# Performance work log

Measured on AMD Instinct MI355X. Metric: run time of the kernel, lower is better.

## Reference

```python
import jax, jax.numpy as jnp
import numpy as np

MODEL_DIM = 1024
NUM_HEADS = 8
DIM_PER_HEAD = MODEL_DIM // NUM_HEADS  # 128
BATCH = 4
NODE_LEN = 128  # must equal DIM_PER_HEAD (see v += relative_mul broadcast in source)
LN_EPS = 1e-5


def setup_inputs() -> dict:
    key0 = jax.random.key(0)
    ks = jax.random.split(key0, 16)
    def w(k, shape, s=0.02):
        return jax.random.normal(k, shape, dtype=jnp.float32) * s
    inp = {
        "key": jax.random.normal(ks[0], (BATCH, NODE_LEN, MODEL_DIM), dtype=jnp.float32),
        "value": jax.random.normal(ks[1], (BATCH, NODE_LEN, MODEL_DIM), dtype=jnp.float32),
        "query": jax.random.normal(ks[2], (BATCH, NODE_LEN, MODEL_DIM), dtype=jnp.float32),
        "relative_q": jax.random.normal(ks[3], (BATCH * NUM_HEADS, NODE_LEN, NODE_LEN, DIM_PER_HEAD), dtype=jnp.float32),
        "relative_v": jax.random.normal(ks[4], (BATCH * NUM_HEADS, NODE_LEN, NODE_LEN, DIM_PER_HEAD), dtype=jnp.float32),
        "Wq": w(ks[5], (MODEL_DIM, MODEL_DIM)), "bq": w(ks[6], (MODEL_DIM,)),
        "Wk": w(ks[7], (MODEL_DIM, MODEL_DIM)), "bk": w(ks[8], (MODEL_DIM,)),
        "Wv": w(ks[9], (MODEL_DIM, MODEL_DIM)), "bv": w(ks[10], (MODEL_DIM,)),
        "Wo": w(ks[11], (MODEL_DIM, MODEL_DIM)), "bo": w(ks[12], (MODEL_DIM,)),
        "ln_gamma": jnp.ones((MODEL_DIM,), dtype=jnp.float32),
        "ln_beta": jnp.zeros((MODEL_DIM,), dtype=jnp.float32),
    }
    return inp


def _relative_mul(x, rel):
    # x: [BH, L, d], rel: [BH, L, L, d] -> [BH, L, L]
    # result[b,i,j] = sum_d x[b,i,d] * rel[b,i,j,d]  (matches torch bmm chain)
    return jnp.einsum('bid,bijd->bij', x, rel)


def reference(key, value, query, relative_q, relative_v,
              Wq, bq, Wk, bk, Wv, bv, Wo, bo, ln_gamma, ln_beta):
    residual = query
    B = key.shape[0]
    H, d = NUM_HEADS, DIM_PER_HEAD

    k = key @ Wk.T + bk      # [B, L, model_dim]
    v = value @ Wv.T + bv
    q = query @ Wq.T + bq

    # faithful to torch .view(batch*heads, -1, dim_per_head): row-major reshape
    k = k.reshape(B * H, -1, d)  # [BH, L, d]
    v = v.reshape(B * H, -1, d)
    q = q.reshape(B * H, -1, d)

    # scale = (dim_per_head // num_heads) ** -0.5, as in source
    scale = (d // H) ** (-0.5)

    attn = jnp.einsum('bid,bjd->bij', q, k)           # [BH, L, L]
    attn = attn + _relative_mul(q, relative_q)
    attn = attn * scale
    attn = jax.nn.softmax(attn, axis=2)

    # source: v += relative_mul(v, relative_v); requires L == d
    v = v + _relative_mul(v, relative_v)              # [BH, L, d] (L == d)
    context = jnp.einsum('bij,bjd->bid', attn, v)     # [BH, L, d]
    context = context.reshape(B, -1, H * d)           # [B, L, model_dim]

    out = context @ Wo.T + bo
    out = out + residual
    mu = jnp.mean(out, axis=-1, keepdims=True)
    var = jnp.mean(jnp.square(out - mu), axis=-1, keepdims=True)
    out = (out - mu) * jax.lax.rsqrt(var + LN_EPS) * ln_gamma + ln_beta
    return (out, attn)
```

## Files before the change

### kernel.cpp

```cpp
#include <hip/hip_runtime.h>

#define MD 1024
#define L 128
#define LN_EPS 1e-5f

typedef __attribute__((ext_vector_type(8))) short bh8;
typedef __attribute__((ext_vector_type(4))) float fx4;
typedef __attribute__((ext_vector_type(4))) float f4;

__device__ __forceinline__ unsigned short f2bf(float x) {
  unsigned int u = __float_as_uint(x);
  u = (u + 0x7FFFu + ((u >> 16) & 1u)) >> 16;
  return (unsigned short)u;
}

__global__ __launch_bounds__(256) void cvt_bf16(
    const float* s0, const float* s1, const float* s2, const float* s3,
    const float* s4, const float* s5, const float* s6, unsigned short* d0,
    unsigned short* d1, unsigned short* d2, unsigned short* d3,
    unsigned short* d4, unsigned short* d5, unsigned short* d6) {
  const float* s;
  unsigned short* d;
  int n;
  switch (blockIdx.z) {
    case 0: s = s0; d = d0; n = 524288; break;
    case 1: s = s1; d = d1; n = 524288; break;
    case 2: s = s2; d = d2; n = 524288; break;
    case 3: s = s3; d = d3; n = 1048576; break;
    case 4: s = s4; d = d4; n = 1048576; break;
    case 5: s = s5; d = d5; n = 1048576; break;
    default: s = s6; d = d6; n = 1048576; break;
  }
  const int idx = (blockIdx.x * 256 + threadIdx.x) * 8;
  if (idx < n) {
    const float4 a = *(const float4*)&s[idx];
    const float4 b = *(const float4*)&s[idx + 4];
    uint4 o;
    o.x = (unsigned int)f2bf(a.x) | ((unsigned int)f2bf(a.y) << 16);
    o.y = (unsigned int)f2bf(a.z) | ((unsigned int)f2bf(a.w) << 16);
    o.z = (unsigned int)f2bf(b.x) | ((unsigned int)f2bf(b.y) << 16);
    o.w = (unsigned int)f2bf(b.z) | ((unsigned int)f2bf(b.w) << 16);
    *(uint4*)&d[idx] = o;
  }
}

__device__ __forceinline__ void mfma_gemm_body(
    const unsigned short* __restrict__ A, const unsigned short* __restrict__ W,
    const float* __restrict__ bias, float* __restrict__ out,
    unsigned short* __restrict__ outb) {
  __shared__ short As[64][40];
  __shared__ short Bs[64][40];
  const int t = threadIdx.x;
  const int row0 = blockIdx.x * 64;
  const int col0 = blockIdx.y * 64;
  const int l = t & 63;
  const int w = t >> 6;
  const int wr = (w >> 1) * 32;
  const int wc = (w & 1) * 32;
  const int srow = t >> 2;
  const int skg = (t & 3) * 8;
  const int fr = l & 15;
  const int fq = (l >> 4) * 8;

  fx4 z = {0.f, 0.f, 0.f, 0.f};
  fx4 acc[2][2];
  acc[0][0] = z; acc[0][1] = z; acc[1][0] = z; acc[1][1] = z;

  for (int k0 = 0; k0 < MD; k0 += 32) {
    const uint4 av = *(const uint4*)&A[(size_t)(row0 + srow) * MD + k0 + skg];
    const uint4 bv = *(const uint4*)&W[(size_t)(col0 + srow) * MD + k0 + skg];
    __syncthreads();
    *(uint4*)&As[srow][skg] = av;
    *(uint4*)&Bs[srow][skg] = bv;
    __syncthreads();
    const bh8 a0 = *(const bh8*)&As[wr + fr][fq];
    const bh8 a1 = *(const bh8*)&As[wr + 16 + fr][fq];
    const bh8 b0 = *(const bh8*)&Bs[wc + fr][fq];
    const bh8 b1 = *(const bh8*)&Bs[wc + 16 + fr][fq];
    acc[0][0] = __builtin_amdgcn_mfma_f32_16x16x32_bf16(a0, b0, acc[0][0], 0, 0, 0);
    acc[0][1] = __builtin_amdgcn_mfma_f32_16x16x32_bf16(a0, b1, acc[0][1], 0, 0, 0);
    acc[1][0] = __builtin_amdgcn_mfma_f32_16x16x32_bf16(a1, b0, acc[1][0], 0, 0, 0);
    acc[1][1] = __builtin_amdgcn_mfma_f32_16x16x32_bf16(a1, b1, acc[1][1], 0, 0, 0);
  }

  const int fq4 = (l >> 4) * 4;
#pragma unroll
  for (int m = 0; m < 2; m++)
#pragma unroll
    for (int n = 0; n < 2; n++) {
      const int col = col0 + wc + n * 16 + fr;
      const float bval = bias[col];
#pragma unroll
      for (int r = 0; r < 4; r++) {
        const int row = row0 + wr + m * 16 + fq4 + r;
        const float v = acc[m][n][r] + bval;
        if (out) out[(size_t)row * MD + col] = v;
        if (outb) outb[(size_t)row * MD + col] = f2bf(v);
      }
    }
}

__global__ __launch_bounds__(256) void qkv_mfma(
    const unsigned short* Aq, const unsigned short* Ak,
    const unsigned short* Av, const unsigned short* Wq,
    const unsigned short* Wk, const unsigned short* Wv, const float* bq,
    const float* bk, const float* bv, float* qo, float* ko, float* vo,
    unsigned short* qb, unsigned short* kb) {
  if (blockIdx.z == 0) mfma_gemm_body(Aq, Wq, bq, qo, qb);
  else if (blockIdx.z == 1) mfma_gemm_body(Ak, Wk, bk, ko, kb);
  else mfma_gemm_body(Av, Wv, bv, vo, nullptr);
}

__global__ __launch_bounds__(256) void o_mfma(const unsigned short* A,
                                              const unsigned short* W,
                                              const float* bias, float* out) {
  mfma_gemm_body(A, W, bias, out, nullptr);
}

__global__ __launch_bounds__(256) void qk_mfma(const unsigned short* __restrict__ qb,
                                               const unsigned short* __restrict__ kb,
                                               float* __restrict__ S1) {
  __shared__ short Qs[128][40];
  __shared__ short Ks[128][40];
  const int g = blockIdx.x;
  const int t = threadIdx.x;
  const int l = t & 63;
  const int w = t >> 6;
  const unsigned short* qg = qb + (size_t)g * 16384;
  const unsigned short* kg = kb + (size_t)g * 16384;
  const int srow = t >> 1;
  const int sh = (t & 1) * 16;
  const int fr = l & 15;
  const int fq = (l >> 4) * 8;

  fx4 z = {0.f, 0.f, 0.f, 0.f};
  fx4 acc[2][8];
#pragma unroll
  for (int m = 0; m < 2; m++)
#pragma unroll
    for (int n = 0; n < 8; n++) acc[m][n] = z;

  for (int d0 = 0; d0 < 128; d0 += 32) {
    const size_t off = (size_t)srow * 128 + d0 + sh;
    const uint4 q0 = *(const uint4*)&qg[off];
    const uint4 q1 = *(const uint4*)&qg[off + 8];
    const uint4 k0 = *(const uint4*)&kg[off];
    const uint4 k1 = *(const uint4*)&kg[off + 8];
    __syncthreads();
    *(uint4*)&Qs[srow][sh] = q0;
    *(uint4*)&Qs[srow][sh + 8] = q1;
    *(uint4*)&Ks[srow][sh] = k0;
    *(uint4*)&Ks[srow][sh + 8] = k1;
    __syncthreads();
    const bh8 a0 = *(const bh8*)&Qs[w * 32 + fr][fq];
    const bh8 a1 = *(const bh8*)&Qs[w * 32 + 16 + fr][fq];
#pragma unroll
    for (int n = 0; n < 8; n++) {
      const bh8 b = *(const bh8*)&Ks[n * 16 + fr][fq];
      acc[0][n] = __builtin_amdgcn_mfma_f32_16x16x32_bf16(a0, b, acc[0][n], 0, 0, 0);
      acc[1][n] = __builtin_amdgcn_mfma_f32_16x16x32_bf16(a1, b, acc[1][n], 0, 0, 0);
    }
  }

  const int fq4 = (l >> 4) * 4;
#pragma unroll
  for (int m = 0; m < 2; m++)
#pragma unroll
    for (int n = 0; n < 8; n++)
#pragma unroll
      for (int r = 0; r < 4; r++) {
        const int i = w * 32 + m * 16 + fq4 + r;
        S1[((size_t)g * 128 + i) * 128 + n * 16 + fr] = acc[m][n][r];
      }
}

__global__ __launch_bounds__(256) void rel_fused(
    const float* __restrict__ q, const float* __restrict__ v,
    const float* __restrict__ rq, const float* __restrict__ rv,
    const float* __restrict__ S1, float* __restrict__ attn,
    float* __restrict__ v2) {
  const int g = blockIdx.x;
  const int i = blockIdx.y;
  const int t = threadIdx.x;
  const int w = t >> 6;
  const int l = t & 63;
  const int c = t & 31;
  const int rlow = t >> 5;

  __shared__ float logits[L];
  __shared__ float vacc_s[L];

  const size_t gi = (size_t)g * L + i;
  const f4 qf = *(const f4*)&q[gi * 128 + c * 4];
  const f4 vf = *(const f4*)&v[gi * 128 + c * 4];

  const f4* rqp = (const f4*)(rq + gi * 16384);
  const f4* rvp = (const f4*)(rv + gi * 16384);

  float aq[16], av[16];
#pragma unroll
  for (int k = 0; k < 16; k++) {
    const f4 d = rqp[t + 256 * k];
    aq[k] = qf.x * d.x + qf.y * d.y + qf.z * d.z + qf.w * d.w;
  }
#pragma unroll
  for (int k = 0; k < 16; k++) {
    const f4 d = __builtin_nontemporal_load(&rvp[t + 256 * k]);
    av[k] = vf.x * d.x + vf.y * d.y + vf.z * d.z + vf.w * d.w;
  }

#pragma unroll
  for (int mask = 1; mask <= 16; mask <<= 1) {
#pragma unroll
    for (int k = 0; k < 16; k++) {
      aq[k] += __shfl_xor(aq[k], mask);
      av[k] += __shfl_xor(av[k], mask);
    }
  }
  if (c == 0) {
#pragma unroll
    for (int k = 0; k < 16; k++) {
      const int row = 8 * k + rlow;
      logits[row] = aq[k];
      vacc_s[row] = av[k];
    }
  }

  __syncthreads();
  if (w == 0) {
    const float* S1p = S1 + gi * 128;
    const float x0 = (logits[l] + S1p[l]) * 0.25f;
    const float x1 = (logits[l + 64] + S1p[l + 64]) * 0.25f;
    float m = fmaxf(x0, x1);
#pragma unroll
    for (int mask = 1; mask <= 32; mask <<= 1) m = fmaxf(m, __shfl_xor(m, mask));
    const float e0 = __expf(x0 - m);
    const float e1 = __expf(x1 - m);
    float ssum = e0 + e1;
#pragma unroll
    for (int mask = 1; mask <= 32; mask <<= 1) ssum += __shfl_xor(ssum, mask);
    const float inv = 1.0f / ssum;
    attn[gi * 128 + l] = e0 * inv;
    attn[gi * 128 + l + 64] = e1 * inv;
  }
  if (t < 128) v2[gi * 128 + t] = v[gi * 128 + t] + vacc_s[t];
}

__global__ __launch_bounds__(256) void context_k(const float* __restrict__ attn,
                                                 const float* __restrict__ v2,
                                                 unsigned short* __restrict__ ctxb) {
  const int g = blockIdx.x;
  const int i = blockIdx.y;
  const int t = threadIdx.x;
  const int dd = t & 127;
  const int h = t >> 7;
  __shared__ float arow[L];
  __shared__ float part[128];
  const size_t gi = (size_t)g * L + i;
  if (t < L) arow[t] = attn[gi * 128 + t];
  __syncthreads();
  float acc = 0.f;
  const float* v2g = v2 + (size_t)g * (L * 128);
#pragma unroll 8
  for (int j = h * 64; j < h * 64 + 64; j++)
    acc = fmaf(arow[j], v2g[j * 128 + dd], acc);
  if (h == 1) part[dd] = acc;
  __syncthreads();
  if (h == 0) ctxb[gi * 128 + dd] = f2bf(acc + part[dd]);
}

__global__ __launch_bounds__(256) void resid_ln(const float* __restrict__ pre,
                                                const float* __restrict__ resid,
                                                const float* __restrict__ gamma,
                                                const float* __restrict__ beta,
                                                float* __restrict__ out) {
  const int r = blockIdx.x;
  const int t = threadIdx.x;
  const float4 p = *(const float4*)&pre[(size_t)r * MD + t * 4];
  const float4 rs = *(const float4*)&resid[(size_t)r * MD + t * 4];
  float4 x;
  x.x = p.x + rs.x; x.y = p.y + rs.y; x.z = p.z + rs.z; x.w = p.w + rs.w;
  float s = x.x + x.y + x.z + x.w;
  float ss = x.x * x.x + x.y * x.y + x.z * x.z + x.w * x.w;
#pragma unroll
  for (int mask = 1; mask <= 32; mask <<= 1) {
    s += __shfl_xor(s, mask);
    ss += __shfl_xor(ss, mask);
  }
  __shared__ float as_[4], aq_[4];
  const int w = t >> 6;
  if ((t & 63) == 0) { as_[w] = s; aq_[w] = ss; }
  __syncthreads();
  s = as_[0] + as_[1] + as_[2] + as_[3];
  ss = aq_[0] + aq_[1] + aq_[2] + aq_[3];
  const float mu = s * (1.0f / 1024.0f);
  const float var = ss * (1.0f / 1024.0f) - mu * mu;
  const float inv = rsqrtf(var + LN_EPS);
  const float4 g4 = *(const float4*)&gamma[t * 4];
  const float4 b4 = *(const float4*)&beta[t * 4];
  float4 o;
  o.x = (x.x - mu) * inv * g4.x + b4.x;
  o.y = (x.y - mu) * inv * g4.y + b4.y;
  o.z = (x.z - mu) * inv * g4.z + b4.z;
  o.w = (x.w - mu) * inv * g4.w + b4.w;
  *(float4*)&out[(size_t)r * MD + t * 4] = o;
}

extern "C" void kernel_launch(void* const* d_in, const int* in_sizes, int n_in,
                              void* d_out, int out_size, void* d_ws,
                              size_t ws_size, hipStream_t stream) {
  (void)in_sizes; (void)n_in; (void)out_size; (void)ws_size;
  const float* key = (const float*)d_in[0];
  const float* value = (const float*)d_in[1];
  const float* query = (const float*)d_in[2];
  const float* rq = (const float*)d_in[3];
  const float* rv = (const float*)d_in[4];
  const float* Wq = (const float*)d_in[5];
  const float* bq = (const float*)d_in[6];
  const float* Wk = (const float*)d_in[7];
  const float* bk = (const float*)d_in[8];
  const float* Wv = (const float*)d_in[9];
  const float* bv = (const float*)d_in[10];
  const float* Wo = (const float*)d_in[11];
  const float* bo = (const float*)d_in[12];
  const float* gamma = (const float*)d_in[13];
  const float* beta = (const float*)d_in[14];

  float* out0 = (float*)d_out;
  float* attn_out = (float*)d_out + 524288;

  float* ws = (float*)d_ws;
  float* q_ws = ws;
  float* k_ws = ws + 524288;
  float* v_ws = ws + 2 * 524288;
  float* v2_ws = ws + 3 * 524288;
  float* pre_ws = ws + 4 * 524288;
  float* S1_ws = ws + 5 * 524288;
  unsigned short* us = (unsigned short*)(ws + 6 * 524288);
  unsigned short* qb = us;
  unsigned short* kb = us + 524288;
  unsigned short* inqb = us + 2 * 524288;
  unsigned short* inkb = us + 3 * 524288;
  unsigned short* invb = us + 4 * 524288;
  unsigned short* ctxb = us + 5 * 524288;
  unsigned short* Wqb = us + 6 * 524288;
  unsigned short* Wkb = Wqb + 1048576;
  unsigned short* Wvb = Wkb + 1048576;
  unsigned short* Wob = Wvb + 1048576;

  cvt_bf16<<<dim3(512, 1, 7), 256, 0, stream>>>(query, key, value, Wq, Wk, Wv,
                                                Wo, inqb, inkb, invb, Wqb, Wkb,
                                                Wvb, Wob);
  qkv_mfma<<<dim3(8, 16, 3), 256, 0, stream>>>(inqb, inkb, invb, Wqb, Wkb, Wvb,
                                               bq, bk, bv, q_ws, k_ws, v_ws,
                                               qb, kb);
  qk_mfma<<<32, 256, 0, stream>>>(qb, kb, S1_ws);
  rel_fused<<<dim3(32, 128), 256, 0, stream>>>(q_ws, v_ws, rq, rv, S1_ws,
                                               attn_out, v2_ws);
  context_k<<<dim3(32, 128), 256, 0, stream>>>(attn_out, v2_ws, ctxb);
  o_mfma<<<dim3(8, 16), 256, 0, stream>>>(ctxb, Wob, bo, pre_ws);
  resid_ln<<<512, 256, 0, stream>>>(pre_ws, query, gamma, beta, out0);
}
```

Before: 151.4 us.

## Stream relative_q/v rows through LDS via async global_load_lds double buffering

Replaces the per-thread register loads of the relative_q and relative_v rows in rel_fused with a double-buffered pipeline. Each wave asynchronously copies 8-row chunks straight into LDS with global_load_lds and waits on vmcnt before reducing. This overlaps the streaming of the large relative tensors with the dot-product and shuffle reductions and lowers register pressure. It adds 32KB of LDS per block, which can reduce occupancy, and relies on per-wave waitcnt ordering without a block barrier.

```diff
diff --git a/kernel.cpp b/kernel.cpp
--- a/kernel.cpp
+++ b/kernel.cpp
@@ -185,8 +185,9 @@
   const int w = t >> 6;
   const int l = t & 63;
   const int c = t & 31;
-  const int rlow = t >> 5;
-
+  const int half = l >> 5;
+
+  __shared__ float buf[2][4096];
   __shared__ float logits[L];
   __shared__ float vacc_s[L];
 
@@ -194,35 +195,53 @@
   const f4 qf = *(const f4*)&q[gi * 128 + c * 4];
   const f4 vf = *(const f4*)&v[gi * 128 + c * 4];
 
-  const f4* rqp = (const f4*)(rq + gi * 16384);
-  const f4* rvp = (const f4*)(rv + gi * 16384);
-
-  float aq[16], av[16];
-#pragma unroll
-  for (int k = 0; k < 16; k++) {
-    const f4 d = rqp[t + 256 * k];
-    aq[k] = qf.x * d.x + qf.y * d.y + qf.z * d.z + qf.w * d.w;
-  }
-#pragma unroll
-  for (int k = 0; k < 16; k++) {
-    const f4 d = __builtin_nontemporal_load(&rvp[t + 256 * k]);
-    av[k] = vf.x * d.x + vf.y * d.y + vf.z * d.z + vf.w * d.w;
-  }
-
-#pragma unroll
-  for (int mask = 1; mask <= 16; mask <<= 1) {
-#pragma unroll
-    for (int k = 0; k < 16; k++) {
-      aq[k] += __shfl_xor(aq[k], mask);
-      av[k] += __shfl_xor(av[k], mask);
-    }
-  }
-  if (c == 0) {
-#pragma unroll
-    for (int k = 0; k < 16; k++) {
-      const int row = 8 * k + rlow;
-      logits[row] = aq[k];
-      vacc_s[row] = av[k];
+  const float* rqp = rq + gi * 16384;
+  const float* rvp = rv + gi * 16384;
+
+  auto stage = [&](int ch) {
+    const float* src = (ch < 4) ? rqp : rvp;
+    const float* sbase = src + ((size_t)((ch & 3) * 32 + w * 8)) * 128;
+    float* dbase = &buf[ch & 1][w * 8 * 128];
+#pragma unroll
+    for (int it = 0; it < 4; it++) {
+      __builtin_amdgcn_global_load_lds(
+          (const __attribute__((address_space(1))) unsigned int*)(sbase + it * 256 + l * 4),
+          (__attribute__((address_space(3))) unsigned int*)(dbase + it * 256),
+          16, 0, 0);
+    }
+  };
+
+  stage(0);
+  stage(1);
+#pragma unroll
+  for (int ch = 0; ch < 8; ch++) {
+    if (ch < 7) {
+      asm volatile("s_waitcnt vmcnt(4)" ::: "memory");
+    } else {
+      asm volatile("s_waitcnt vmcnt(0)" ::: "memory");
+    }
+    __builtin_amdgcn_sched_barrier(0);
+    const float* bp = &buf[ch & 1][w * 8 * 128];
+    float acc[4];
+#pragma unroll
+    for (int it = 0; it < 4; it++) {
+      const f4 d = *(const f4*)&bp[it * 256 + l * 4];
+      const f4 f = (ch < 4) ? qf : vf;
+      acc[it] = f.x * d.x + f.y * d.y + f.z * d.z + f.w * d.w;
+    }
+    __builtin_amdgcn_sched_barrier(0);
+    if (ch + 2 < 8) stage(ch + 2);
+#pragma unroll
+    for (int mask = 1; mask <= 16; mask <<= 1)
+#pragma unroll
+      for (int it = 0; it < 4; it++) acc[it] += __shfl_xor(acc[it], mask);
+    if (c == 0) {
+#pragma unroll
+      for (int it = 0; it < 4; it++) {
+        const int j = (ch & 3) * 32 + w * 8 + it * 2 + half;
+        if (ch < 4) logits[j] = acc[it];
+        else vacc_s[j] = acc[it];
+      }
     }
   }
 
```

Result: slower. 171.3 us (+13.2%).
